# Optimization experiments

Hardware: AMD Instinct MI355X
Metric: run time of the kernel (lower is better)

The kernel has to match this reference:

```python
import jax, jax.numpy as jnp
import numpy as np
from jax import lax

HEADS = 4
FH = FW = FD = 4
LN_EPS = 1e-5
NORM_EPS = 1e-12


def setup_inputs() -> dict:
    key = jax.random.key(0)
    k0, k1, k2 = jax.random.split(key, 3)
    B, H, W, D, C = 1, 64, 64, 64, 96
    x = jax.random.normal(k0, (B, H, W, D, C), jnp.float32)
    ln_gamma = jnp.ones((C,), jnp.float32)
    ln_beta = jnp.zeros((C,), jnp.float32)
    # Conv3d(C, 3C, k=3, pad=1) kernel in DHWIO layout
    qkv_w = jax.random.normal(k1, (3, 3, 3, C, 3 * C), jnp.float32) * 0.02
    qkv_b = jnp.zeros((3 * C,), jnp.float32)
    # torch Linear weight [out, in]
    out_w = jax.random.normal(k2, (C, C), jnp.float32) * 0.02
    out_b = jnp.zeros((C,), jnp.float32)
    temperature = jnp.ones((HEADS, 1, 1), jnp.float32)
    return {"x": x, "ln_gamma": ln_gamma, "ln_beta": ln_beta,
            "qkv_w": qkv_w, "qkv_b": qkv_b,
            "out_w": out_w, "out_b": out_b, "temperature": temperature}


def _l2norm(t):
    # torch F.normalize(dim=-1, eps=1e-12)
    n = jnp.linalg.norm(t, axis=-1, keepdims=True)
    return t / jnp.maximum(n, NORM_EPS)


def reference(x, ln_gamma, ln_beta, qkv_w, qkv_b, out_w, out_b, temperature):
    B, H, W, D, C = x.shape
    gh, gw, gd = H // FH, W // FW, D // FD  # 64x64x64 divisible -> no padding
    G, F = gh * gw * gd, FH * FW * FD
    ch = C // HEADS
    shortcut = x

    # LayerNorm over channels
    mu = jnp.mean(x, axis=-1, keepdims=True)
    var = jnp.var(x, axis=-1, keepdims=True)
    xn = (x - mu) * lax.rsqrt(var + LN_EPS) * ln_gamma + ln_beta

    # conv3d QKV projection (kernel 3, stride 1, SAME padding)
    y = lax.conv_general_dilated(
        xn, qkv_w, window_strides=(1, 1, 1), padding='SAME',
        dimension_numbers=('NDHWC', 'DHWIO', 'NDHWC')) + qkv_b

    # split volume into regions: [B, G, F, 3C]
    y = y.reshape(B, gh, FH, gw, FW, gd, FD, 3 * C)
    y = y.transpose(0, 1, 3, 5, 2, 4, 6, 7).reshape(B, G, F, 3 * C)
    q, k, v = jnp.split(y, 3, axis=-1)

    def to_heads(t):  # b g f (head c) -> b f head c g
        return t.reshape(B, G, F, HEADS, ch).transpose(0, 2, 3, 4, 1)

    q, k, v = to_heads(q), to_heads(k), to_heads(v)
    q, k = _l2norm(q), _l2norm(k)

    # channel x channel attention per (batch, intra-region pos, head)
    attn = jnp.einsum('bfhcg,bfhdg->bfhcd', q, k) * temperature
    attn = jax.nn.softmax(attn, axis=-1)
    out = jnp.einsum('bfhcd,bfhdg->bfhcg', attn, v)

    # b f head c g -> b g f (head c)
    out = out.transpose(0, 4, 1, 2, 3).reshape(B, G, F, C)
    out = out @ out_w.T + out_b

    # regions back to volume
    out = out.reshape(B, gh, gw, gd, FH, FW, FD, C)
    out = out.transpose(0, 1, 4, 2, 5, 3, 6, 7).reshape(B, H, W, D, C)
    return out + shortcut
```

## Files before the change

### kernel.cpp

```cpp
#include <hip/hip_runtime.h>
#include <stdint.h>

typedef unsigned short u16;
typedef float f32x4 __attribute__((ext_vector_type(4)));
typedef float f32x16 __attribute__((ext_vector_type(16)));
typedef __bf16 v8bf __attribute__((ext_vector_type(8)));

static __device__ __forceinline__ float bf2f(u16 u) {
  union { uint32_t i; float f; } v; v.i = ((uint32_t)u) << 16; return v.f;
}
static __device__ __forceinline__ u16 f2bf(float f) {
  union { float f; uint32_t i; } v; v.f = f;
  uint32_t b = v.i;
  return (u16)((b + 0x7FFFu + ((b >> 16) & 1u)) >> 16);
}

__global__ __launch_bounds__(256) void k_ln(const float* __restrict__ x,
                                            const float* __restrict__ gamma,
                                            const float* __restrict__ beta,
                                            u16* __restrict__ xn) {
  int tid = threadIdx.x;
  int vox = blockIdx.x * 64 + (tid >> 2);
  int q = tid & 3;
  const float4* px = (const float4*)(x + (size_t)vox * 96 + q * 24);
  float f[24];
  *(float4*)&f[0]  = px[0]; *(float4*)&f[4]  = px[1]; *(float4*)&f[8]  = px[2];
  *(float4*)&f[12] = px[3]; *(float4*)&f[16] = px[4]; *(float4*)&f[20] = px[5];
  float s = 0.f, s2 = 0.f;
#pragma unroll
  for (int i = 0; i < 24; ++i) { s += f[i]; s2 += f[i] * f[i]; }
  s += __shfl_xor(s, 1);  s += __shfl_xor(s, 2);
  s2 += __shfl_xor(s2, 1); s2 += __shfl_xor(s2, 2);
  float mu = s * (1.f / 96.f);
  float var = s2 * (1.f / 96.f) - mu * mu;
  float rs = rsqrtf(var + 1e-5f);
  uint32_t ow[12];
#pragma unroll
  for (int i = 0; i < 12; ++i) {
    int c0 = q * 24 + 2 * i;
    float v0 = (f[2 * i]     - mu) * rs * gamma[c0]     + beta[c0];
    float v1 = (f[2 * i + 1] - mu) * rs * gamma[c0 + 1] + beta[c0 + 1];
    ow[i] = (uint32_t)f2bf(v0) | ((uint32_t)f2bf(v1) << 16);
  }
  uint4* po = (uint4*)(xn + (size_t)vox * 96 + q * 24);
  po[0] = *(uint4*)&ow[0]; po[1] = *(uint4*)&ow[4]; po[2] = *(uint4*)&ow[8];
}

__global__ __launch_bounds__(256) void k_repack(const float* __restrict__ qw,
                                                u16* __restrict__ Wb) {
  int t = blockIdx.x * 256 + threadIdx.x;
  if (t >= 27 * 3 * 18 * 64) return;
  int l = t & 63;
  int rest = t >> 6;
  int nt = rest % 18;
  int ks = (rest / 18) % 3;
  int tap = rest / 54;
  int co = nt * 16 + (l & 15);
  int cibase = ks * 32 + (l >> 4) * 8;
  u16 vals[8];
#pragma unroll
  for (int j = 0; j < 8; ++j)
    vals[j] = f2bf(qw[((size_t)tap * 96 + cibase + j) * 288 + co]);
  *(uint4*)(Wb + (size_t)t * 8) = *(uint4*)vals;
}

__global__ __launch_bounds__(256, 2) void k_conv(const u16* __restrict__ xn,
                                                 const u16* __restrict__ Wb,
                                                 const float* __restrict__ qkvb,
                                                 u16* __restrict__ y) {
  __shared__ u16 As[2][2 * 66 * 104];
  int tid = threadIdx.x;
  int bid = blockIdx.x;
  int swz = (bid & 7) * 256 + (bid >> 3);
  int x0 = swz >> 5;
  int y0 = (swz & 31) * 2;
  int lane = tid & 63, w = tid >> 6;
  int wcol = w >> 1, wc = w & 1;

  f32x4 acc[4][9];
#pragma unroll
  for (int m = 0; m < 4; ++m)
#pragma unroll
    for (int n = 0; n < 9; ++n) acc[m][n] = (f32x4)0.f;

  const u16* wbase = Wb + (size_t)(wc * 9) * 512 + (size_t)lane * 8;

#define STAGE_A(DXY, BUF)                                                      \
  {                                                                            \
    int dx_ = (DXY) / 3, dy_ = (DXY) % 3;                                      \
    int xx_ = x0 + dx_ - 1;                                                    \
    for (int i = tid; i < 2 * 66 * 12; i += 256) {                             \
      int c_ = i / 792, rem_ = i - c_ * 792;                                   \
      int row_ = rem_ / 12, c8_ = rem_ - row_ * 12;                            \
      int yy_ = y0 + c_ + dy_ - 1;                                             \
      uint4 v_ = make_uint4(0u, 0u, 0u, 0u);                                   \
      if (((unsigned)xx_ < 64u) && ((unsigned)yy_ < 64u) && row_ >= 1 &&       \
          row_ <= 64) {                                                        \
        const uint4* src_ = (const uint4*)(xn + ((size_t)(xx_ * 64 + yy_) * 64) * 96); \
        v_ = src_[(row_ - 1) * 12 + c8_];                                      \
      }                                                                        \
      *(uint4*)&As[BUF][(c_ * 66 + row_) * 104 + c8_ * 8] = v_;                \
    }                                                                          \
  }

  STAGE_A(0, 0);
  __syncthreads();

  v8bf b[9];
#pragma unroll
  for (int nt = 0; nt < 9; ++nt)
    b[nt] = *(const v8bf*)(wbase + (size_t)nt * 512);

  for (int dxy = 0; dxy < 9; ++dxy) {
    const u16* Ab = &As[dxy & 1][0];
    const u16* base2 = wbase + (size_t)dxy * 9 * 9216;
    bool last_dxy = (dxy == 8);

#pragma unroll
    for (int t = 0; t < 9; ++t) {
      int dz = t / 3, ks = t - dz * 3;
      int ar = (lane & 15) + dz;
      int ac = ks * 32 + (lane >> 4) * 8;
      const u16* abase = &Ab[(wcol * 66 + ar) * 104 + ac];
      v8bf a0 = *(const v8bf*)(abase);
      v8bf a1 = *(const v8bf*)(abase + 16 * 104);
      v8bf a2 = *(const v8bf*)(abase + 32 * 104);
      v8bf a3 = *(const v8bf*)(abase + 48 * 104);
      const u16* bnxt = base2 + (size_t)(t + 1) * 9216;
      bool more = (t < 8) || !last_dxy;
      __builtin_amdgcn_s_setprio(1);
#pragma unroll
      for (int nt = 0; nt < 9; ++nt) {
        v8bf bb = b[nt];
        acc[0][nt] = __builtin_amdgcn_mfma_f32_16x16x32_bf16(a0, bb, acc[0][nt], 0, 0, 0);
        acc[1][nt] = __builtin_amdgcn_mfma_f32_16x16x32_bf16(a1, bb, acc[1][nt], 0, 0, 0);
        acc[2][nt] = __builtin_amdgcn_mfma_f32_16x16x32_bf16(a2, bb, acc[2][nt], 0, 0, 0);
        acc[3][nt] = __builtin_amdgcn_mfma_f32_16x16x32_bf16(a3, bb, acc[3][nt], 0, 0, 0);
        if (more) b[nt] = *(const v8bf*)(bnxt + (size_t)nt * 512);
      }
      __builtin_amdgcn_s_setprio(0);
    }

    if (!last_dxy) STAGE_A(dxy + 1, (dxy + 1) & 1);
    __syncthreads();
  }
#undef STAGE_A

  size_t voxbase = ((size_t)x0 * 64 + (y0 + wcol)) * 64;
#pragma unroll
  for (int m = 0; m < 4; ++m)
#pragma unroll
    for (int nt = 0; nt < 9; ++nt) {
      int co = wc * 144 + nt * 16 + (lane & 15);
      float bias = qkvb[co];
#pragma unroll
      for (int r = 0; r < 4; ++r) {
        int vrow = m * 16 + (lane >> 4) * 4 + r;
        y[(voxbase + vrow) * 288 + co] = f2bf(acc[m][nt][r] + bias);
      }
    }
}

__global__ __launch_bounds__(256) void k_gram2(const u16* __restrict__ y,
                                               float* __restrict__ S_part,
                                               float* __restrict__ qn_part,
                                               float* __restrict__ kn_part) {
  __shared__ u16 buf[2][16 * 292];
  int tid = threadIdx.x;
  int f = blockIdx.x >> 4, chunk = blockIdx.x & 15;
  int fx = f >> 4, fy = (f >> 2) & 3, fz = f & 3;
  int l = tid & 63, h = tid >> 6;

  f32x16 aqk = (f32x16)0.f, aqq = (f32x16)0.f, akk = (f32x16)0.f;

  int i0 = tid;
  int gl0 = i0 / 24, c80 = i0 - gl0 * 24;
  int c00 = c80 * 8;
  int dst0 = (c00 < 96) ? ((c00 / 24) * 32 + (c00 % 24))
                        : (128 + ((c00 - 96) / 24) * 32 + ((c00 - 96) % 24));
  int i1 = tid + 256;
  int gl1 = i1 / 24, c81 = i1 - gl1 * 24;
  int c01 = c81 * 8;
  int dst1 = (c01 < 96) ? ((c01 / 24) * 32 + (c01 % 24))
                        : (128 + ((c01 - 96) / 24) * 32 + ((c01 - 96) % 24));
  bool has1 = (tid < 128);

  uint4 s0, s1;
  auto gload = [&](int sub) {
    int gbase = chunk * 256 + sub * 16;
    {
      int g = gbase + gl0;
      int gx = g >> 8, gy = (g >> 4) & 15, gz = g & 15;
      size_t vox = ((size_t)(gx * 4 + fx) * 64 + (gy * 4 + fy)) * 64 + (gz * 4 + fz);
      s0 = *(const uint4*)(y + vox * 288 + c00);
    }
    if (has1) {
      int g = gbase + gl1;
      int gx = g >> 8, gy = (g >> 4) & 15, gz = g & 15;
      size_t vox = ((size_t)(gx * 4 + fx) * 64 + (gy * 4 + fy)) * 64 + (gz * 4 + fz);
      s1 = *(const uint4*)(y + vox * 288 + c01);
    }
  };
  auto gwrite = [&](int bufi) {
    u16* p0 = &buf[bufi][gl0 * 292 + dst0];
    *(uint2*)p0 = make_uint2(s0.x, s0.y);
    *(uint2*)(p0 + 4) = make_uint2(s0.z, s0.w);
    if (has1) {
      u16* p1 = &buf[bufi][gl1 * 292 + dst1];
      *(uint2*)p1 = make_uint2(s1.x, s1.y);
      *(uint2*)(p1 + 4) = make_uint2(s1.z, s1.w);
    }
  };

  gload(0);
  gwrite(0);
  __syncthreads();

  for (int sub = 0; sub < 16; ++sub) {
    if (sub < 15) gload(sub + 1);
    const u16* bb = &buf[sub & 1][(l >> 5) * 8 * 292 + h * 32 + (l & 31)];
    v8bf aq, ak;
#pragma unroll
    for (int j = 0; j < 8; ++j) {
      ((u16*)&aq)[j] = bb[j * 292];
      ((u16*)&ak)[j] = bb[j * 292 + 128];
    }
    aqk = __builtin_amdgcn_mfma_f32_32x32x16_bf16(aq, ak, aqk, 0, 0, 0);
    aqq = __builtin_amdgcn_mfma_f32_32x32x16_bf16(aq, aq, aqq, 0, 0, 0);
    akk = __builtin_amdgcn_mfma_f32_32x32x16_bf16(ak, ak, akk, 0, 0, 0);
    if (sub < 15) gwrite((sub + 1) & 1);
    __syncthreads();
  }

  int col = l & 31, hi = l >> 5;
  if (col < 24) {
    float* Sp = S_part + (((size_t)(chunk * 64 + f)) * 4 + h) * 576;
#pragma unroll
    for (int reg = 0; reg < 12; ++reg) {
      int row = (reg & 3) + 8 * (reg >> 2) + 4 * hi;
      Sp[row * 24 + col] = aqk[reg];
    }
    int sel = (col & 7) - 4 * hi;
    if (sel >= 0 && sel < 4) {
      int dreg = (col >> 3) * 4 + sel;
      float qn = 0.f, kn = 0.f;
#pragma unroll
      for (int r = 0; r < 12; ++r)
        if (r == dreg) { qn = aqq[r]; kn = akk[r]; }
      qn_part[((size_t)(chunk * 64 + f)) * 96 + h * 24 + col] = qn;
      kn_part[((size_t)(chunk * 64 + f)) * 96 + h * 24 + col] = kn;
    }
  }
}

__global__ __launch_bounds__(256) void k_attn(const float* __restrict__ S_part,
                                              const float* __restrict__ qn_part,
                                              const float* __restrict__ kn_part,
                                              const float* __restrict__ out_w,
                                              const float* __restrict__ temp,
                                              u16* __restrict__ Mtf) {
  __shared__ float Ssum[2304];
  __shared__ float attn[2304];
  __shared__ float invq[96], invk[96];
  __shared__ float ow[9216];
  int tid = threadIdx.x;
  int f = blockIdx.x;
  for (int o = tid; o < 2304; o += 256) {
    float s = 0.f;
#pragma unroll
    for (int c = 0; c < 16; ++c) s += S_part[((size_t)(c * 64 + f)) * 2304 + o];
    Ssum[o] = s;
  }
  if (tid < 96) {
    float qn = 0.f, kn = 0.f;
#pragma unroll
    for (int c = 0; c < 16; ++c) {
      qn += qn_part[((size_t)(c * 64 + f)) * 96 + tid];
      kn += kn_part[((size_t)(c * 64 + f)) * 96 + tid];
    }
    invq[tid] = 1.f / fmaxf(sqrtf(qn), 1e-12f);
    invk[tid] = 1.f / fmaxf(sqrtf(kn), 1e-12f);
  }
  for (int i = tid; i < 9216; i += 256) ow[i] = out_w[i];
  __syncthreads();
  if (tid < 96) {
    int h = tid / 24, c = tid % 24;
    float tmp = temp[h];
    const float* Sr = &Ssum[h * 576 + c * 24];
    float lg[24];
    float mx = -1e30f;
#pragma unroll
    for (int d = 0; d < 24; ++d) {
      lg[d] = Sr[d] * invq[tid] * invk[h * 24 + d] * tmp;
      mx = fmaxf(mx, lg[d]);
    }
    float sum = 0.f;
#pragma unroll
    for (int d = 0; d < 24; ++d) { lg[d] = __expf(lg[d] - mx); sum += lg[d]; }
    float inv = 1.f / sum;
#pragma unroll
    for (int d = 0; d < 24; ++d) attn[h * 576 + c * 24 + d] = lg[d] * inv;
  }
  __syncthreads();
  for (int o = tid; o < 9216; o += 256) {
    int j = o / 96, cp = o - j * 96;
    int h2 = j / 24, d = j % 24;
    float s = 0.f;
#pragma unroll
    for (int cc = 0; cc < 24; ++cc)
      s += attn[h2 * 576 + cc * 24 + d] * ow[cp * 96 + h2 * 24 + cc];
    int ks = j >> 5, rem = j & 31;
    int lane = ((rem >> 3) << 4) + (cp & 15);
    int nt = cp >> 4, e = rem & 7;
    Mtf[(((size_t)f * 18 + ks * 6 + nt) * 64 + lane) * 8 + e] = f2bf(s);
  }
}

__global__ __launch_bounds__(256) void k_final2(const u16* __restrict__ y,
                                                const u16* __restrict__ Mtf,
                                                const float* __restrict__ xin,
                                                const float* __restrict__ out_b,
                                                float* __restrict__ out) {
  __shared__ u16 vst[4 * 16 * 104];
  int tid = threadIdx.x;
  int b = blockIdx.x;
  int x = b >> 6, yy = b & 63;
  size_t colvox = ((size_t)x * 64 + yy) * 64;
  int l = tid & 63, w = tid >> 6;
  int fx = x & 3, fy = yy & 3;
  const u16* mtb = Mtf + ((size_t)(fx * 16 + fy * 4 + w) * 18) * 512 + (size_t)l * 8;

  for (int i = tid; i < 768; i += 256) {
    int vv = i / 12, c8 = i - vv * 12;
    *(uint4*)&vst[((vv & 3) * 16 + (vv >> 2)) * 104 + c8 * 8] =
        *(const uint4*)(y + (colvox + vv) * 288 + 192 + c8 * 8);
  }
  __syncthreads();

  f32x4 acc[6];
#pragma unroll
  for (int nt = 0; nt < 6; ++nt) acc[nt] = (f32x4)0.f;

#pragma unroll
  for (int ks = 0; ks < 3; ++ks) {
    v8bf a = *(const v8bf*)&vst[(w * 16 + (l & 15)) * 104 + ks * 32 + (l >> 4) * 8];
#pragma unroll
    for (int nt = 0; nt < 6; ++nt) {
      v8bf bb = *(const v8bf*)(mtb + (size_t)(ks * 6 + nt) * 512);
      acc[nt] = __builtin_amdgcn_mfma_f32_16x16x32_bf16(a, bb, acc[nt], 0, 0, 0);
    }
  }

#pragma unroll
  for (int nt = 0; nt < 6; ++nt) {
    int cp = nt * 16 + (l & 15);
    float ob = out_b[cp];
#pragma unroll
    for (int r = 0; r < 4; ++r) {
      int vox = w + 4 * ((l >> 4) * 4 + r);
      size_t idx = (colvox + vox) * 96 + cp;
      out[idx] = acc[nt][r] + ob + xin[idx];
    }
  }
}

extern "C" void kernel_launch(void* const* d_in, const int* in_sizes, int n_in,
                              void* d_out, int out_size, void* d_ws, size_t ws_size,
                              hipStream_t stream) {
  const float* x  = (const float*)d_in[0];
  const float* g  = (const float*)d_in[1];
  const float* be = (const float*)d_in[2];
  const float* qw = (const float*)d_in[3];
  const float* qb = (const float*)d_in[4];
  const float* ow = (const float*)d_in[5];
  const float* ob = (const float*)d_in[6];
  const float* tp = (const float*)d_in[7];
  float* out = (float*)d_out;

  u16* xn = (u16*)d_out;
  float* S_part  = (float*)((char*)d_out + 50331648);
  float* qn_part = (float*)((char*)d_out + 59768832);
  float* kn_part = (float*)((char*)d_out + 60162048);

  char* w = (char*)d_ws;
  u16* y   = (u16*)(w);
  u16* Wb  = (u16*)(w + 150994944);
  u16* Mtf = (u16*)(w + 152487936);

  hipLaunchKernelGGL(k_ln, dim3(4096), dim3(256), 0, stream, x, g, be, xn);
  hipLaunchKernelGGL(k_repack, dim3((27 * 3 * 18 * 64 + 255) / 256), dim3(256), 0, stream, qw, Wb);
  hipLaunchKernelGGL(k_conv, dim3(2048), dim3(256), 0, stream, xn, Wb, qb, y);
  hipLaunchKernelGGL(k_gram2, dim3(1024), dim3(256), 0, stream, y, S_part, qn_part, kn_part);
  hipLaunchKernelGGL(k_attn, dim3(64), dim3(256), 0, stream, S_part, qn_part, kn_part, ow, tp, Mtf);
  hipLaunchKernelGGL(k_final2, dim3(4096), dim3(256), 0, stream, y, Mtf, x, ob, out);
}
```

Before: 476.8 us.

## Stage four y-columns per x-plane to reuse halo across dy taps

The conv kernel now loads four y-columns (including the halo) of the input slab into shared memory once per dx offset, instead of reloading two columns for every (dx,dy) pair. The three dy taps read shifted rows from the same buffer, so global-to-LDS staging and barrier rounds drop from nine to three per block. In exchange, double buffering is gone: each restage is bracketed by barriers with no overlap against MFMA work. The single buffer is the same size as the old pair, so occupancy should be unchanged.

```diff
diff --git a/kernel.cpp b/kernel.cpp
--- a/kernel.cpp
+++ b/kernel.cpp
@@ -68,7 +68,7 @@
                                                  const u16* __restrict__ Wb,
                                                  const float* __restrict__ qkvb,
                                                  u16* __restrict__ y) {
-  __shared__ u16 As[2][2 * 66 * 104];
+  __shared__ u16 As[4 * 66 * 104];
   int tid = threadIdx.x;
   int bid = blockIdx.x;
   int swz = (bid & 7) * 256 + (bid >> 3);
@@ -85,49 +85,49 @@
 
   const u16* wbase = Wb + (size_t)(wc * 9) * 512 + (size_t)lane * 8;
 
-#define STAGE_A(DXY, BUF)                                                      \
+#define STAGE_A(DX)                                                            \
   {                                                                            \
-    int dx_ = (DXY) / 3, dy_ = (DXY) % 3;                                      \
-    int xx_ = x0 + dx_ - 1;                                                    \
-    for (int i = tid; i < 2 * 66 * 12; i += 256) {                             \
+    int xx_ = x0 + (DX) - 1;                                                   \
+    for (int i = tid; i < 4 * 66 * 12; i += 256) {                             \
       int c_ = i / 792, rem_ = i - c_ * 792;                                   \
       int row_ = rem_ / 12, c8_ = rem_ - row_ * 12;                            \
-      int yy_ = y0 + c_ + dy_ - 1;                                             \
+      int yy_ = y0 + c_ - 1;                                                   \
       uint4 v_ = make_uint4(0u, 0u, 0u, 0u);                                   \
       if (((unsigned)xx_ < 64u) && ((unsigned)yy_ < 64u) && row_ >= 1 &&       \
           row_ <= 64) {                                                        \
         const uint4* src_ = (const uint4*)(xn + ((size_t)(xx_ * 64 + yy_) * 64) * 96); \
         v_ = src_[(row_ - 1) * 12 + c8_];                                      \
       }                                                                        \
-      *(uint4*)&As[BUF][(c_ * 66 + row_) * 104 + c8_ * 8] = v_;                \
+      *(uint4*)&As[(c_ * 66 + row_) * 104 + c8_ * 8] = v_;                     \
     }                                                                          \
   }
 
-  STAGE_A(0, 0);
-  __syncthreads();
+  STAGE_A(0);
 
   v8bf b[9];
 #pragma unroll
   for (int nt = 0; nt < 9; ++nt)
     b[nt] = *(const v8bf*)(wbase + (size_t)nt * 512);
 
-  for (int dxy = 0; dxy < 9; ++dxy) {
-    const u16* Ab = &As[dxy & 1][0];
-    const u16* base2 = wbase + (size_t)dxy * 9 * 9216;
-    bool last_dxy = (dxy == 8);
-
-#pragma unroll
-    for (int t = 0; t < 9; ++t) {
-      int dz = t / 3, ks = t - dz * 3;
+  __syncthreads();
+
+  for (int dx = 0; dx < 3; ++dx) {
+    const u16* base2 = wbase + (size_t)dx * 27 * 9216;
+    bool last_dx = (dx == 2);
+
+#pragma unroll
+    for (int t2 = 0; t2 < 27; ++t2) {
+      int dy = t2 / 9, rem9 = t2 - dy * 9;
+      int dz = rem9 / 3, ks = rem9 - dz * 3;
       int ar = (lane & 15) + dz;
       int ac = ks * 32 + (lane >> 4) * 8;
-      const u16* abase = &Ab[(wcol * 66 + ar) * 104 + ac];
+      const u16* abase = &As[((wcol + dy) * 66 + ar) * 104 + ac];
       v8bf a0 = *(const v8bf*)(abase);
       v8bf a1 = *(const v8bf*)(abase + 16 * 104);
       v8bf a2 = *(const v8bf*)(abase + 32 * 104);
       v8bf a3 = *(const v8bf*)(abase + 48 * 104);
-      const u16* bnxt = base2 + (size_t)(t + 1) * 9216;
-      bool more = (t < 8) || !last_dxy;
+      const u16* bnxt = base2 + (size_t)(t2 + 1) * 9216;
+      bool more = (t2 < 26) || !last_dx;
       __builtin_amdgcn_s_setprio(1);
 #pragma unroll
       for (int nt = 0; nt < 9; ++nt) {
@@ -141,8 +141,11 @@
       __builtin_amdgcn_s_setprio(0);
     }
 
-    if (!last_dxy) STAGE_A(dxy + 1, (dxy + 1) & 1);
-    __syncthreads();
+    if (!last_dx) {
+      __syncthreads();
+      STAGE_A(dx + 1);
+      __syncthreads();
+    }
   }
 #undef STAGE_A
 
```

Measured after the change: 452.9 us, median of 2. -5.0%, faster.
